# Kernel optimization log

Measured on AMD Instinct MI355X. Metric: run time of the kernel, lower is better.

The kernel has to match this reference:

```python
import jax, jax.numpy as jnp
import numpy as np

SCALE = 1.0 / (100.0 ** 0.5)  # module hard-codes QK / sqrt(100)


def setup_inputs() -> dict:
    key = jax.random.key(0)
    k1, k2, k3 = jax.random.split(key, 3)
    B, S, D = 8, 2048, 512
    head_size = 64
    x = jax.random.normal(k1, (B, S, D), dtype=jnp.float32)
    kernel = jax.random.normal(k2, (3, D, head_size), dtype=jnp.float32) * 0.02
    dense = jax.random.normal(k3, (D, D), dtype=jnp.float32) * 0.02
    return {"x": x, "kernel": kernel, "dense": dense, "heads": 8}


def reference(x, kernel, dense, heads):
    # All heads use the SAME kernel slices in the original loop, so each
    # iteration produces an identical V; compute once and tile.
    WQ = jnp.einsum('bsd,dh->bsh', x, kernel[0])  # [B,S,Hd]
    WK = jnp.einsum('bsd,dh->bsh', x, kernel[1])
    WV = jnp.einsum('bsd,dh->bsh', x, kernel[2])
    scores = jnp.einsum('bqh,bkh->bqk', WQ, WK) * SCALE  # [B,S,S]
    attn = jax.nn.softmax(scores, axis=-1)
    V = jnp.einsum('bqk,bkh->bqh', attn, WV)  # [B,S,Hd]
    out = jnp.tile(V, (1, 1, heads))  # concat of identical heads -> [B,S,heads*Hd]
    return jnp.einsum('bsf,fo->bso', out, dense)
```

## Files before the change

kernel.cpp:

```cpp
#include <hip/hip_runtime.h>
#include <math.h>


typedef __bf16 bf16;
typedef __bf16 bf16x4v __attribute__((ext_vector_type(4)));
typedef __bf16 bf16x8v __attribute__((ext_vector_type(8)));
typedef float f32x4 __attribute__((ext_vector_type(4)));

namespace {
constexpr int kS = 2048;
constexpr int kD = 512;
constexpr int kRows = 16384;
}

#define MFMA16(a, b, c) __builtin_amdgcn_mfma_f32_16x16x32_bf16((a), (b), (c), 0, 0, 0)

__global__ __launch_bounds__(256) void prep_kernel(const float* __restrict__ w,
                                                   const float* __restrict__ dense,
                                                   bf16* __restrict__ wtg,
                                                   bf16* __restrict__ drt) {
  int idx = blockIdx.x * 256 + threadIdx.x;
  if (idx < 98304) {
    int mat = idx >> 15, rem = idx & 32767;
    int n = rem >> 9, k = rem & 511;
    wtg[idx] = (bf16)w[mat * 32768 + k * 64 + n];
  } else {
    int e = idx - 98304;
    int o = e >> 6, j = e & 63;
    float s = 0.f;
#pragma unroll
    for (int h = 0; h < 8; ++h) s += dense[(size_t)(h * 64 + j) * kD + o];
    drt[e] = (bf16)s;
  }
}

__global__ __launch_bounds__(256) void proj_kernel(const float* __restrict__ x,
                                                   const bf16* __restrict__ wtg,
                                                   bf16* __restrict__ wq,
                                                   bf16* __restrict__ wk,
                                                   bf16* __restrict__ wvt) {
  const int bt = blockIdx.x;
  const int tid = threadIdx.x;
  const int w = tid >> 6, tx = tid & 15, quad = (tid >> 4) & 3;
  const int row0 = bt * 64;

  __shared__ bf16 Xs[64 * 72];
  __shared__ bf16 Wts[3 * 64 * 72];

  f32x4 acc[3][4];
#pragma unroll
  for (int m = 0; m < 3; ++m)
#pragma unroll
    for (int nt = 0; nt < 4; ++nt) acc[m][nt] = (f32x4){0.f, 0.f, 0.f, 0.f};

  for (int k0 = 0; k0 < kD; k0 += 64) {
    __syncthreads();
#pragma unroll
    for (int p = 0; p < 4; ++p) {
      int i4 = tid + p * 256;
      int r = i4 >> 4, c4 = (i4 & 15) * 4;
      float4 f = *(const float4*)&x[(size_t)(row0 + r) * kD + k0 + c4];
      bf16x4v h = {(bf16)f.x, (bf16)f.y, (bf16)f.z, (bf16)f.w};
      *(bf16x4v*)&Xs[r * 72 + c4] = h;
    }
#pragma unroll
    for (int p = 0; p < 6; ++p) {
      int cc = tid + p * 256;
      int mat = cc >> 9, rem = cc & 511;
      int n = rem >> 3, c8 = (rem & 7) * 8;
      *(uint4*)&Wts[(mat * 64 + n) * 72 + c8] =
          *(const uint4*)&wtg[(size_t)mat * 32768 + (size_t)n * 512 + k0 + c8];
    }
    __syncthreads();
#pragma unroll
    for (int s = 0; s < 2; ++s) {
      bf16x8v a = *(bf16x8v*)&Xs[(w * 16 + tx) * 72 + s * 32 + quad * 8];
#pragma unroll
      for (int m = 0; m < 3; ++m)
#pragma unroll
        for (int nt = 0; nt < 4; ++nt) {
          bf16x8v bfr =
              *(bf16x8v*)&Wts[(m * 64 + nt * 16 + tx) * 72 + s * 32 + quad * 8];
          acc[m][nt] = MFMA16(a, bfr, acc[m][nt]);
        }
    }
  }

#pragma unroll
  for (int nt = 0; nt < 4; ++nt)
#pragma unroll
    for (int r = 0; r < 4; ++r) {
      int row_g = row0 + w * 16 + quad * 4 + r;
      int col = nt * 16 + tx;
      wq[(size_t)row_g * 64 + col] = (bf16)acc[0][nt][r];
      wk[(size_t)row_g * 64 + col] = (bf16)acc[1][nt][r];
    }
  __syncthreads();
  bf16* Vt = Xs;
#pragma unroll
  for (int nt = 0; nt < 4; ++nt)
#pragma unroll
    for (int r = 0; r < 4; ++r)
      Vt[(nt * 16 + tx) * 72 + (w * 16 + quad * 4 + r)] = (bf16)acc[2][nt][r];
  __syncthreads();
#pragma unroll
  for (int p = 0; p < 2; ++p) {
    int c = tid + p * 256;
    int v = c >> 3, seg = c & 7;
    *(uint4*)&wvt[(size_t)v * kRows + row0 + seg * 8] =
        *(uint4*)&Vt[v * 72 + seg * 8];
  }
}

__global__ __launch_bounds__(512, 4) void flash_kernel(
    const bf16* __restrict__ wq, const bf16* __restrict__ wk,
    const bf16* __restrict__ wvt, const bf16* __restrict__ drt,
    float* __restrict__ out) {
  const int bid = blockIdx.x;
  const int b = bid & 7, qb = bid >> 3;
  const int q0 = qb * 32;
  const int tid = threadIdx.x;
  const int w = tid >> 6, lane = tid & 63, tx = tid & 15, quad = (tid >> 4) & 3;

  __shared__ __align__(16) char lds[65536];
  __shared__ float Lsh[256];
  __shared__ __align__(16) bf16 vob[32 * 64];
  bf16* Ksw = (bf16*)(lds + w * 8192);
  bf16* Psw = Ksw;
  bf16* Vtw = (bf16*)(lds + w * 8192 + 4096);

  const bf16* wqb = wq + (size_t)(b * kS) * 64;
  const bf16* wkb = wk + (size_t)(b * kS) * 64;
  const bf16* wvb = wvt + b * kS;

  const int kc0 = (quad ^ (tx & 7)) * 8;
  const int kc1 = ((4 + quad) ^ (tx & 7)) * 8;
  const int h2 = (tx ^ (tx >> 2)) & 3;

  bf16x8v aq[2][2];
#pragma unroll
  for (int rt = 0; rt < 2; ++rt)
#pragma unroll
    for (int s = 0; s < 2; ++s)
      aq[rt][s] = *(const bf16x8v*)&wqb[(size_t)(q0 + rt * 16 + tx) * 64 +
                                        s * 32 + quad * 8];

  f32x4 oacc[2][4];
#pragma unroll
  for (int rt = 0; rt < 2; ++rt)
#pragma unroll
    for (int nt = 0; nt < 4; ++nt) oacc[rt][nt] = (f32x4){0.f, 0.f, 0.f, 0.f};
  float lsum[2][4] = {};

  const int ksr = lane >> 3, kslc = lane & 7;
  const int vsv = lane >> 2, vsck = lane & 3;

  for (int t = 0; t < 8; ++t) {
    const int k0 = (t * 8 + w) * 32;
#pragma unroll
    for (int j = 0; j < 4; ++j) {
      int r = ksr + j * 8;
      *(uint4*)&Ksw[r * 64 + ((kslc ^ (r & 7)) * 8)] =
          *(const uint4*)&wkb[(size_t)(k0 + r) * 64 + kslc * 8];
      int v = vsv + j * 16;
      *(uint4*)&Vtw[v * 32 + ((vsck ^ ((v ^ (v >> 2)) & 3)) * 8)] =
          *(const uint4*)&wvb[(size_t)v * kRows + k0 + vsck * 8];
    }

#pragma unroll
    for (int nt = 0; nt < 2; ++nt) {
      int krow = nt * 16 + tx;
      bf16x8v b0 = *(bf16x8v*)&Ksw[krow * 64 + kc0];
      bf16x8v b1 = *(bf16x8v*)&Ksw[krow * 64 + kc1];
#pragma unroll
      for (int rt = 0; rt < 2; ++rt) {
        f32x4 z = (f32x4){0.f, 0.f, 0.f, 0.f};
        z = MFMA16(aq[rt][0], b0, z);
        z = MFMA16(aq[rt][1], b1, z);
#pragma unroll
        for (int r = 0; r < 4; ++r) {
          float p = __expf(z[r] * 0.1f);
          lsum[rt][r] += p;
          int q = rt * 16 + quad * 4 + r;
          int chunk = nt * 2 + (tx >> 3);
          Psw[q * 32 + ((chunk ^ (r ^ quad)) * 8) + (tx & 7)] = (bf16)p;
        }
      }
    }

#pragma unroll
    for (int rt = 0; rt < 2; ++rt) {
      bf16x8v pa = *(bf16x8v*)&Psw[(rt * 16 + tx) * 32 + ((quad ^ h2) * 8)];
#pragma unroll
      for (int nt = 0; nt < 4; ++nt) {
        bf16x8v vb = *(bf16x8v*)&Vtw[(nt * 16 + tx) * 32 + ((quad ^ h2) * 8)];
        oacc[rt][nt] = MFMA16(pa, vb, oacc[rt][nt]);
      }
    }
  }

  __syncthreads();
  float* myO = (float*)(lds + w * 8192);
  float* myL = Lsh + w * 32;
#pragma unroll
  for (int rt = 0; rt < 2; ++rt)
#pragma unroll
    for (int nt = 0; nt < 4; ++nt)
#pragma unroll
      for (int r = 0; r < 4; ++r)
        myO[(rt * 16 + quad * 4 + r) * 64 + nt * 16 + tx] = oacc[rt][nt][r];
#pragma unroll
  for (int rt = 0; rt < 2; ++rt)
#pragma unroll
    for (int r = 0; r < 4; ++r) {
      float v = lsum[rt][r];
#pragma unroll
      for (int m = 1; m < 16; m <<= 1) v += __shfl_xor(v, m, 64);
      if (tx == 0) myL[rt * 16 + quad * 4 + r] = v;
    }
  __syncthreads();

#pragma unroll
  for (int p = 0; p < 4; ++p) {
    int e = tid + p * 512;
    int row = e >> 6, col = e & 63;
    float s = 0.f, lt = 0.f;
#pragma unroll
    for (int wv = 0; wv < 8; ++wv) {
      s += ((const float*)(lds + wv * 8192))[e];
      lt += Lsh[wv * 32 + row];
    }
    vob[row * 64 + (((col >> 3) ^ (row & 7)) * 8) + (col & 7)] = (bf16)(s / lt);
  }
  __syncthreads();

  bf16x8v av[2][2];
#pragma unroll
  for (int rt = 0; rt < 2; ++rt) {
    av[rt][0] = *(bf16x8v*)&vob[(rt * 16 + tx) * 64 + kc0];
    av[rt][1] = *(bf16x8v*)&vob[(rt * 16 + tx) * 64 + kc1];
  }

  float* OutS = (float*)lds;
#pragma unroll
  for (int c = 0; c < 2; ++c) {
    if (c) __syncthreads();
#pragma unroll
    for (int i = 0; i < 2; ++i) {
      const int ct = c * 16 + w * 2 + i;
      bf16x8v bd0 =
          *(const bf16x8v*)&drt[(size_t)(ct * 16 + tx) * 64 + quad * 8];
      bf16x8v bd1 =
          *(const bf16x8v*)&drt[(size_t)(ct * 16 + tx) * 64 + 32 + quad * 8];
#pragma unroll
      for (int rt = 0; rt < 2; ++rt) {
        f32x4 z = (f32x4){0.f, 0.f, 0.f, 0.f};
        z = MFMA16(av[rt][0], bd0, z);
        z = MFMA16(av[rt][1], bd1, z);
#pragma unroll
        for (int r = 0; r < 4; ++r)
          OutS[(rt * 16 + quad * 4 + r) * 260 + (w * 2 + i) * 16 + tx] = z[r];
      }
    }
    __syncthreads();
#pragma unroll
    for (int p = 0; p < 4; ++p) {
      int e = tid + p * 512;
      int row = e >> 6, seg = e & 63;
      *(float4*)&out[(size_t)(b * kS + q0 + row) * kD + c * 256 + seg * 4] =
          *(float4*)&OutS[row * 260 + seg * 4];
    }
  }
}

extern "C" void kernel_launch(void* const* d_in, const int* in_sizes, int n_in,
                              void* d_out, int out_size, void* d_ws,
                              size_t ws_size, hipStream_t stream) {
  const float* x = (const float*)d_in[0];
  const float* w = (const float*)d_in[1];
  const float* dense = (const float*)d_in[2];
  float* out = (float*)d_out;

  bf16* wq = (bf16*)d_ws;
  bf16* wk = wq + (size_t)kRows * 64;
  bf16* wvt = wk + (size_t)kRows * 64;
  bf16* wtg = wvt + (size_t)kRows * 64;
  bf16* drt = wtg + 98304;

  prep_kernel<<<512, 256, 0, stream>>>(w, dense, wtg, drt);
  proj_kernel<<<256, 256, 0, stream>>>(x, wtg, wq, wk, wvt);
  flash_kernel<<<512, 512, 0, stream>>>(wq, wk, wvt, drt, out);
}
```

Baseline: 138.4 us.

## Halve query tile per block, load K fragments directly, shrink LDS for occupancy

The flash kernel now processes 16 query rows per block instead of 32 and launches twice as many blocks. K fragments are read straight from global memory into registers instead of being staged through LDS, and the shared-memory footprint drops from roughly 74KB to 40KB so more blocks can be resident per CU. The aim is better occupancy and latency hiding across the 256 CUs. In exchange, each block re-reads all of K and V for half as many queries, doubling global and L2 traffic for K/V and the dense weights.

Result: slower. 153.0 us (+10.5%).

```diff
diff --git a/kernel.cpp b/kernel.cpp
--- a/kernel.cpp
+++ b/kernel.cpp
@@ -112,22 +112,19 @@
   }
 }
 
-__global__ __launch_bounds__(512, 4) void flash_kernel(
+__global__ __launch_bounds__(512, 8) void flash_kernel(
     const bf16* __restrict__ wq, const bf16* __restrict__ wk,
     const bf16* __restrict__ wvt, const bf16* __restrict__ drt,
     float* __restrict__ out) {
   const int bid = blockIdx.x;
   const int b = bid & 7, qb = bid >> 3;
-  const int q0 = qb * 32;
+  const int q0 = qb * 16;
   const int tid = threadIdx.x;
   const int w = tid >> 6, lane = tid & 63, tx = tid & 15, quad = (tid >> 4) & 3;
 
-  __shared__ __align__(16) char lds[65536];
-  __shared__ float Lsh[256];
-  __shared__ __align__(16) bf16 vob[32 * 64];
-  bf16* Ksw = (bf16*)(lds + w * 8192);
-  bf16* Psw = Ksw;
-  bf16* Vtw = (bf16*)(lds + w * 8192 + 4096);
+  __shared__ __align__(16) char lds[40960];
+  bf16* Vtw = (bf16*)(lds + w * 5120);
+  bf16* Psw = (bf16*)(lds + w * 5120 + 4096);
 
   const bf16* wqb = wq + (size_t)(b * kS) * 64;
   const bf16* wkb = wk + (size_t)(b * kS) * 64;
@@ -137,109 +134,93 @@
   const int kc1 = ((4 + quad) ^ (tx & 7)) * 8;
   const int h2 = (tx ^ (tx >> 2)) & 3;
 
-  bf16x8v aq[2][2];
-#pragma unroll
-  for (int rt = 0; rt < 2; ++rt)
-#pragma unroll
-    for (int s = 0; s < 2; ++s)
-      aq[rt][s] = *(const bf16x8v*)&wqb[(size_t)(q0 + rt * 16 + tx) * 64 +
-                                        s * 32 + quad * 8];
-
-  f32x4 oacc[2][4];
-#pragma unroll
-  for (int rt = 0; rt < 2; ++rt)
-#pragma unroll
-    for (int nt = 0; nt < 4; ++nt) oacc[rt][nt] = (f32x4){0.f, 0.f, 0.f, 0.f};
-  float lsum[2][4] = {};
-
-  const int ksr = lane >> 3, kslc = lane & 7;
+  bf16x8v aq0 = *(const bf16x8v*)&wqb[(size_t)(q0 + tx) * 64 + quad * 8];
+  bf16x8v aq1 = *(const bf16x8v*)&wqb[(size_t)(q0 + tx) * 64 + 32 + quad * 8];
+
+  f32x4 oacc[4];
+#pragma unroll
+  for (int nt = 0; nt < 4; ++nt) oacc[nt] = (f32x4){0.f, 0.f, 0.f, 0.f};
+  float lsum[4] = {0.f, 0.f, 0.f, 0.f};
+
   const int vsv = lane >> 2, vsck = lane & 3;
 
   for (int t = 0; t < 8; ++t) {
     const int k0 = (t * 8 + w) * 32;
 #pragma unroll
     for (int j = 0; j < 4; ++j) {
-      int r = ksr + j * 8;
-      *(uint4*)&Ksw[r * 64 + ((kslc ^ (r & 7)) * 8)] =
-          *(const uint4*)&wkb[(size_t)(k0 + r) * 64 + kslc * 8];
       int v = vsv + j * 16;
       *(uint4*)&Vtw[v * 32 + ((vsck ^ ((v ^ (v >> 2)) & 3)) * 8)] =
           *(const uint4*)&wvb[(size_t)v * kRows + k0 + vsck * 8];
     }
-
+    bf16x8v kb[2][2];
 #pragma unroll
     for (int nt = 0; nt < 2; ++nt) {
-      int krow = nt * 16 + tx;
-      bf16x8v b0 = *(bf16x8v*)&Ksw[krow * 64 + kc0];
-      bf16x8v b1 = *(bf16x8v*)&Ksw[krow * 64 + kc1];
-#pragma unroll
-      for (int rt = 0; rt < 2; ++rt) {
-        f32x4 z = (f32x4){0.f, 0.f, 0.f, 0.f};
-        z = MFMA16(aq[rt][0], b0, z);
-        z = MFMA16(aq[rt][1], b1, z);
-#pragma unroll
-        for (int r = 0; r < 4; ++r) {
-          float p = __expf(z[r] * 0.1f);
-          lsum[rt][r] += p;
-          int q = rt * 16 + quad * 4 + r;
-          int chunk = nt * 2 + (tx >> 3);
-          Psw[q * 32 + ((chunk ^ (r ^ quad)) * 8) + (tx & 7)] = (bf16)p;
-        }
+      kb[nt][0] =
+          *(const bf16x8v*)&wkb[(size_t)(k0 + nt * 16 + tx) * 64 + quad * 8];
+      kb[nt][1] = *(const bf16x8v*)&wkb[(size_t)(k0 + nt * 16 + tx) * 64 + 32 +
+                                        quad * 8];
+    }
+
+#pragma unroll
+    for (int nt = 0; nt < 2; ++nt) {
+      f32x4 z = (f32x4){0.f, 0.f, 0.f, 0.f};
+      z = MFMA16(aq0, kb[nt][0], z);
+      z = MFMA16(aq1, kb[nt][1], z);
+#pragma unroll
+      for (int r = 0; r < 4; ++r) {
+        float p = __expf(z[r] * 0.1f);
+        lsum[r] += p;
+        int q = quad * 4 + r;
+        int chunk = nt * 2 + (tx >> 3);
+        Psw[q * 32 + ((chunk ^ (r ^ quad)) * 8) + (tx & 7)] = (bf16)p;
       }
     }
 
-#pragma unroll
-    for (int rt = 0; rt < 2; ++rt) {
-      bf16x8v pa = *(bf16x8v*)&Psw[(rt * 16 + tx) * 32 + ((quad ^ h2) * 8)];
-#pragma unroll
-      for (int nt = 0; nt < 4; ++nt) {
-        bf16x8v vb = *(bf16x8v*)&Vtw[(nt * 16 + tx) * 32 + ((quad ^ h2) * 8)];
-        oacc[rt][nt] = MFMA16(pa, vb, oacc[rt][nt]);
-      }
-    }
-  }
-
-  __syncthreads();
-  float* myO = (float*)(lds + w * 8192);
-  float* myL = Lsh + w * 32;
-#pragma unroll
-  for (int rt = 0; rt < 2; ++rt)
-#pragma unroll
-    for (int nt = 0; nt < 4; ++nt)
-#pragma unroll
-      for (int r = 0; r < 4; ++r)
-        myO[(rt * 16 + quad * 4 + r) * 64 + nt * 16 + tx] = oacc[rt][nt][r];
-#pragma unroll
-  for (int rt = 0; rt < 2; ++rt)
-#pragma unroll
-    for (int r = 0; r < 4; ++r) {
-      float v = lsum[rt][r];
-#pragma unroll
-      for (int m = 1; m < 16; m <<= 1) v += __shfl_xor(v, m, 64);
-      if (tx == 0) myL[rt * 16 + quad * 4 + r] = v;
-    }
-  __syncthreads();
-
-#pragma unroll
-  for (int p = 0; p < 4; ++p) {
+    bf16x8v pa = *(bf16x8v*)&Psw[tx * 32 + ((quad ^ h2) * 8)];
+#pragma unroll
+    for (int nt = 0; nt < 4; ++nt) {
+      bf16x8v vb = *(bf16x8v*)&Vtw[(nt * 16 + tx) * 32 + ((quad ^ h2) * 8)];
+      oacc[nt] = MFMA16(pa, vb, oacc[nt]);
+    }
+  }
+
+  __syncthreads();
+  float* myO = (float*)(lds + w * 5120);
+  float* Lsh = (float*)(lds + 29696);
+#pragma unroll
+  for (int nt = 0; nt < 4; ++nt)
+#pragma unroll
+    for (int r = 0; r < 4; ++r)
+      myO[(quad * 4 + r) * 64 + nt * 16 + tx] = oacc[nt][r];
+#pragma unroll
+  for (int r = 0; r < 4; ++r) {
+    float v = lsum[r];
+#pragma unroll
+    for (int m = 1; m < 16; m <<= 1) v += __shfl_xor(v, m, 64);
+    if (tx == 0) Lsh[w * 16 + quad * 4 + r] = v;
+  }
+  __syncthreads();
+
+#pragma unroll
+  for (int p = 0; p < 2; ++p) {
     int e = tid + p * 512;
     int row = e >> 6, col = e & 63;
     float s = 0.f, lt = 0.f;
 #pragma unroll
     for (int wv = 0; wv < 8; ++wv) {
-      s += ((const float*)(lds + wv * 8192))[e];
-      lt += Lsh[wv * 32 + row];
-    }
-    vob[row * 64 + (((col >> 3) ^ (row & 7)) * 8) + (col & 7)] = (bf16)(s / lt);
-  }
-  __syncthreads();
-
-  bf16x8v av[2][2];
-#pragma unroll
-  for (int rt = 0; rt < 2; ++rt) {
-    av[rt][0] = *(bf16x8v*)&vob[(rt * 16 + tx) * 64 + kc0];
-    av[rt][1] = *(bf16x8v*)&vob[(rt * 16 + tx) * 64 + kc1];
-  }
+      s += ((const float*)(lds + wv * 5120))[e];
+      lt += Lsh[wv * 16 + row];
+    }
+    bf16* vbase = (bf16*)(lds + ((row < 8) ? 34816 : 39936));
+    vbase[(row & 7) * 64 + (((col >> 3) ^ (row & 7)) * 8) + (col & 7)] =
+        (bf16)(s / lt);
+  }
+  __syncthreads();
+
+  const bf16* vbase = (const bf16*)(lds + ((tx < 8) ? 34816 : 39936)) +
+                      (size_t)(tx & 7) * 64;
+  bf16x8v av0 = *(const bf16x8v*)&vbase[kc0];
+  bf16x8v av1 = *(const bf16x8v*)&vbase[kc1];
 
   float* OutS = (float*)lds;
 #pragma unroll
@@ -252,19 +233,16 @@
           *(const bf16x8v*)&drt[(size_t)(ct * 16 + tx) * 64 + quad * 8];
       bf16x8v bd1 =
           *(const bf16x8v*)&drt[(size_t)(ct * 16 + tx) * 64 + 32 + quad * 8];
-#pragma unroll
-      for (int rt = 0; rt < 2; ++rt) {
-        f32x4 z = (f32x4){0.f, 0.f, 0.f, 0.f};
-        z = MFMA16(av[rt][0], bd0, z);
-        z = MFMA16(av[rt][1], bd1, z);
-#pragma unroll
-        for (int r = 0; r < 4; ++r)
-          OutS[(rt * 16 + quad * 4 + r) * 260 + (w * 2 + i) * 16 + tx] = z[r];
-      }
+      f32x4 z = (f32x4){0.f, 0.f, 0.f, 0.f};
+      z = MFMA16(av0, bd0, z);
+      z = MFMA16(av1, bd1, z);
+#pragma unroll
+      for (int r = 0; r < 4; ++r)
+        OutS[(quad * 4 + r) * 260 + (w * 2 + i) * 16 + tx] = z[r];
     }
     __syncthreads();
 #pragma unroll
-    for (int p = 0; p < 4; ++p) {
+    for (int p = 0; p < 2; ++p) {
       int e = tid + p * 512;
       int row = e >> 6, seg = e & 63;
       *(float4*)&out[(size_t)(b * kS + q0 + row) * kD + c * 256 + seg * 4] =
@@ -289,5 +267,5 @@
 
   prep_kernel<<<512, 256, 0, stream>>>(w, dense, wtg, drt);
   proj_kernel<<<256, 256, 0, stream>>>(x, wtg, wq, wk, wvt);
-  flash_kernel<<<512, 512, 0, stream>>>(wq, wk, wvt, drt, out);
-}
+  flash_kernel<<<1024, 512, 0, stream>>>(wq, wk, wvt, drt, out);
+}
```
